# Optimization experiments

Hardware: AMD Instinct MI355X
Metric: run time of the kernel (lower is better)

## Reference

```python
import jax, jax.numpy as jnp
import numpy as np

B, N, D = 4, 2048, 512
H, DA, DL = 8, 64, 64  # heads, attention_dim, linear_dim
EPS = 1e-6


def _layer_norm(x, eps=EPS):
    # F.layer_norm with no affine params
    mu = jnp.mean(x, axis=-1, keepdims=True)
    var = jnp.var(x, axis=-1, keepdims=True)
    return (x - mu) * jax.lax.rsqrt(var + eps)


def setup_inputs() -> dict:
    key = jax.random.key(0)
    k1, k2, k3, k4 = jax.random.split(key, 4)
    x = jax.random.normal(k1, (B, N, D), dtype=jnp.float32)
    # causal (lower-triangular) valid-attention mask, float {0,1}, shape (B,1,N,N)
    attention_mask = jnp.broadcast_to(
        jnp.tril(jnp.ones((N, N), dtype=jnp.float32))[None, None], (B, 1, N, N)
    )
    # _uvqk: (D, 2*H*DL + 2*H*DA), init normal(0, 0.02)
    uvqk = 0.02 * jax.random.normal(k2, (D, 2 * H * DL + 2 * H * DA), dtype=jnp.float32)
    # _o: Linear(H*DL -> D), xavier uniform
    fan_in, fan_out = H * DL, D
    limit = float(np.sqrt(6.0 / (fan_in + fan_out)))
    o_weight = jax.random.uniform(k3, (fan_out, fan_in), dtype=jnp.float32, minval=-limit, maxval=limit)
    o_bias = jnp.zeros((D,), dtype=jnp.float32)
    return {"x": x, "attention_mask": attention_mask, "uvqk": uvqk,
            "o_weight": o_weight, "o_bias": o_bias}


def reference(x, attention_mask, uvqk, o_weight, o_bias):
    b, n, _ = x.shape
    normed_x = _layer_norm(x)
    mm = jax.nn.silu(normed_x @ uvqk)  # fused uvqk projection + silu
    u, v, q, k = jnp.split(mm, [H * DL, 2 * H * DL, 2 * H * DL + H * DA], axis=-1)
    qh = q.reshape(b, n, H, DA)
    kh = k.reshape(b, n, H, DA)
    vh = v.reshape(b, n, H, DL)
    # silu-activated (non-softmax) attention with mask
    qk = jnp.einsum('bnhd,bmhd->bhnm', qh, kh)
    qk = jax.nn.silu(qk) / n
    qk = qk * attention_mask  # (B,1,N,N) broadcast over heads
    attn = jnp.einsum('bhnm,bmhd->bnhd', qk, vh).reshape(b, n, H * DL)
    # gated norm + output proj + residual
    o_input = u * _layer_norm(attn)
    return o_input @ o_weight.T + o_bias + x
```

## Files before the change

### kernel.cpp

```cpp
#include <hip/hip_runtime.h>

typedef __bf16 bf16x8 __attribute__((ext_vector_type(8)));
typedef float f32x4 __attribute__((ext_vector_type(4)));
typedef float f32x16 __attribute__((ext_vector_type(16)));
typedef int i32x2 __attribute__((ext_vector_type(2)));

__device__ __forceinline__ unsigned short f2bf(float f) {
  return __builtin_bit_cast(unsigned short, (__bf16)f);
}
__device__ __forceinline__ float bfu2f(unsigned short b) {
  unsigned int u = ((unsigned int)b) << 16;
  return __builtin_bit_cast(float, u);
}
__device__ __forceinline__ float silu_f(float x) {
  return x * __builtin_amdgcn_rcpf(1.0f + __expf(-x));
}
__device__ __forceinline__ unsigned pk2(float a, float b) {
  return (unsigned)f2bf(a) | ((unsigned)f2bf(b) << 16);
}

template<int CPR, int NI, int SWZ>
__device__ __forceinline__ void stage16(const __bf16* __restrict__ g, int ld,
                                        __bf16* lds, int wave, int lane) {
#pragma unroll
  for (int t = 0; t < NI; ++t) {
    int cb = (wave * NI + t) * 64;
    int c = cb + lane;
    int row = c / CPR;
    int colb = (c % CPR) ^ (row & SWZ);
    __builtin_amdgcn_global_load_lds(
        (const __attribute__((address_space(1))) unsigned int*)(g + row * ld + colb * 8),
        (__attribute__((address_space(3))) unsigned int*)(lds + cb * 8),
        16, 0, 0);
  }
}

__global__ void k_prep(const float* __restrict__ x, __bf16* __restrict__ nx,
                       const float* __restrict__ ow, __bf16* __restrict__ owb,
                       const float* __restrict__ uvqk, __bf16* __restrict__ uvqkT) {
  int bid = blockIdx.x, tid = threadIdx.x;
  if (bid < 4096) {
    int t = tid & 127;
    int r = bid * 2 + (tid >> 7);
    int wave = tid >> 6;
    float4 v = ((const float4*)(x + (size_t)r * 512))[t];
    float s = v.x + v.y + v.z + v.w;
    float ss = v.x * v.x + v.y * v.y + v.z * v.z + v.w * v.w;
#pragma unroll
    for (int o = 32; o > 0; o >>= 1) { s += __shfl_down(s, o); ss += __shfl_down(ss, o); }
    __shared__ float red[4][2];
    if ((tid & 63) == 0) { red[wave][0] = s; red[wave][1] = ss; }
    __syncthreads();
    int rw = (wave >> 1) * 2;
    s = red[rw][0] + red[rw + 1][0];
    ss = red[rw][1] + red[rw + 1][1];
    float mu = s * (1.0f / 512.0f);
    float var = ss * (1.0f / 512.0f) - mu * mu;
    float rs = rsqrtf(var + 1e-6f);
    ushort4 o4;
    o4.x = f2bf((v.x - mu) * rs); o4.y = f2bf((v.y - mu) * rs);
    o4.z = f2bf((v.z - mu) * rs); o4.w = f2bf((v.w - mu) * rs);
    ((ushort4*)(nx + (size_t)r * 512))[t] = o4;
  } else if (bid < 4352) {
    int i = (bid - 4096) * 256 + tid;
    float4 v = ((const float4*)ow)[i];
    ushort4 o4;
    o4.x = f2bf(v.x); o4.y = f2bf(v.y); o4.z = f2bf(v.z); o4.w = f2bf(v.w);
    ((ushort4*)owb)[i] = o4;
  } else {
    __shared__ float tile[32][33];
    int bb = bid - 4352;
    int n0 = (bb & 63) * 32, k0 = (bb >> 6) * 32;
    int tx = tid & 31, ty = tid >> 5;
    for (int i = ty; i < 32; i += 8)
      tile[i][tx] = uvqk[(k0 + i) * 2048 + n0 + tx];
    __syncthreads();
    for (int i = ty; i < 32; i += 8)
      uvqkT[(n0 + i) * 512 + k0 + tx] = (__bf16)tile[tx][i];
  }
}

__global__ __launch_bounds__(256, 2) void k_proj(
    const __bf16* __restrict__ A, const __bf16* __restrict__ Bt,
    __bf16* __restrict__ u, __bf16* __restrict__ qn,
    __bf16* __restrict__ kn, __bf16* __restrict__ vt) {
  __shared__ __bf16 lds[32768];
  int tid = threadIdx.x, wave = tid >> 6, lane = tid & 63;
  int lr = lane & 15, lq = lane >> 4;
  int bn = blockIdx.x, bm = blockIdx.y;
  const __bf16* Ag = A + (size_t)bm * 128 * 512;
  const __bf16* Bg = Bt + (size_t)bn * 128 * 512;
  int wm = (wave >> 1) * 64, wn = (wave & 1) * 64;
  f32x4 acc[4][4] = {};
  stage16<8, 4, 7>(Ag, 512, lds, wave, lane);
  stage16<8, 4, 7>(Bg, 512, lds + 8192, wave, lane);
  asm volatile("s_waitcnt vmcnt(0)" ::: "memory");
  __builtin_amdgcn_sched_barrier(0);
  __builtin_amdgcn_s_barrier();
  __builtin_amdgcn_sched_barrier(0);
  int buf = 0;
  for (int t = 0; t < 8; ++t) {
    if (t + 1 < 8) {
      int nb = buf ^ 1;
      stage16<8, 4, 7>(Ag + (t + 1) * 64, 512, lds + nb * 16384, wave, lane);
      stage16<8, 4, 7>(Bg + (t + 1) * 64, 512, lds + nb * 16384 + 8192, wave, lane);
    }
    const __bf16* As = lds + buf * 16384;
    const __bf16* Bs = lds + buf * 16384 + 8192;
#pragma unroll
    for (int kk = 0; kk < 2; ++kk) {
      int b = kk * 4 + lq;
      bf16x8 a[4], bb[4];
#pragma unroll
      for (int i = 0; i < 4; ++i) {
        int row = wm + i * 16 + lr;
        a[i] = *(const bf16x8*)(As + row * 64 + ((b ^ (row & 7)) * 8));
      }
#pragma unroll
      for (int j = 0; j < 4; ++j) {
        int row = wn + j * 16 + lr;
        bb[j] = *(const bf16x8*)(Bs + row * 64 + ((b ^ (row & 7)) * 8));
      }
#pragma unroll
      for (int i = 0; i < 4; ++i)
#pragma unroll
        for (int j = 0; j < 4; ++j)
          acc[i][j] = __builtin_amdgcn_mfma_f32_16x16x32_bf16(a[i], bb[j], acc[i][j], 0, 0, 0);
    }
    asm volatile("s_waitcnt vmcnt(0)" ::: "memory");
    __builtin_amdgcn_sched_barrier(0);
    __builtin_amdgcn_s_barrier();
    __builtin_amdgcn_sched_barrier(0);
    buf ^= 1;
  }
  int seg = bn >> 2;
  int cb = (bn & 3) * 128 + wn;
  int rb0 = bm * 128 + wm + lq * 4;
  if (seg == 1) {
#pragma unroll
    for (int i = 0; i < 4; ++i) {
      int rb = rb0 + i * 16;
      int b = rb >> 11, n = rb & 2047;
#pragma unroll
      for (int j = 0; j < 4; ++j) {
        int c = cb + j * 16 + lr;
        ushort4 w;
        w.x = f2bf(silu_f(acc[i][j][0]) * (1.0f / 2048.0f));
        w.y = f2bf(silu_f(acc[i][j][1]) * (1.0f / 2048.0f));
        w.z = f2bf(silu_f(acc[i][j][2]) * (1.0f / 2048.0f));
        w.w = f2bf(silu_f(acc[i][j][3]) * (1.0f / 2048.0f));
        *(ushort4*)(vt + ((size_t)(b * 512 + c)) * 2048 + n) = w;
      }
    }
  } else {
    __bf16* dst = (seg == 0) ? u : ((seg == 2) ? qn : kn);
#pragma unroll
    for (int i = 0; i < 4; ++i) {
      int rb = rb0 + i * 16;
#pragma unroll
      for (int j = 0; j < 4; ++j) {
        int c = cb + j * 16 + lr;
#pragma unroll
        for (int rg = 0; rg < 4; ++rg)
          dst[(size_t)(rb + rg) * 512 + c] = (__bf16)silu_f(acc[i][j][rg]);
      }
    }
  }
}

template<bool DT>
__device__ __forceinline__ void attn_finish(
    const f32x16& s, int m0, int n0, int l31, int lh, int ms, bool natural,
    const __bf16* Vc, f32x16 po[2]) {
  unsigned pk[8];
#pragma unroll
  for (int q = 0; q < 8; ++q) {
    float p01[2];
#pragma unroll
    for (int h = 0; h < 2; ++h) {
      int r = 2 * q + h;
      float xx = s[r];
      float pv = xx * __builtin_amdgcn_rcpf(1.0f + __expf(-xx));
      if (DT) {
        int mrow = m0 + 4 * lh + (r & 3) + 8 * (r >> 2);
        if (mrow > n0 + l31) pv = 0.0f;
      }
      p01[h] = pv;
    }
    pk[q] = pk2(p01[0], p01[1]);
  }
  i32x2 r0 = __builtin_amdgcn_permlane32_swap((int)pk[0], (int)pk[2], false, false);
  i32x2 r1 = __builtin_amdgcn_permlane32_swap((int)pk[1], (int)pk[3], false, false);
  i32x2 r2 = __builtin_amdgcn_permlane32_swap((int)pk[4], (int)pk[6], false, false);
  i32x2 r3 = __builtin_amdgcn_permlane32_swap((int)pk[5], (int)pk[7], false, false);
  union { bf16x8 v; unsigned u[4]; } f0, f1;
  if (natural) {
    f0.u[0] = r0.x; f0.u[2] = r0.y; f0.u[1] = r1.x; f0.u[3] = r1.y;
    f1.u[0] = r2.x; f1.u[2] = r2.y; f1.u[1] = r3.x; f1.u[3] = r3.y;
  } else {
    f0.u[0] = r0.y; f0.u[2] = r0.x; f0.u[1] = r1.y; f0.u[3] = r1.x;
    f1.u[0] = r2.y; f1.u[2] = r2.x; f1.u[1] = r3.y; f1.u[3] = r3.x;
  }
  bf16x8 pf[2] = { f0.v, f1.v };
#pragma unroll
  for (int t2 = 0; t2 < 2; ++t2) {
#pragma unroll
    for (int idl = 0; idl < 2; ++idl) {
      int row = idl * 32 + l31;
      bf16x8 av = *(const bf16x8*)(Vc + row * 64 +
          (((ms * 4 + t2 * 2 + lh) ^ (row & 7)) * 8));
      po[idl] = __builtin_amdgcn_mfma_f32_32x32x16_bf16(av, pf[t2], po[idl], 0, 0, 0);
    }
  }
}

__global__ __launch_bounds__(256, 4) void k_attn(
    const __bf16* __restrict__ qn, const __bf16* __restrict__ kn,
    const __bf16* __restrict__ vt, __bf16* __restrict__ oa,
    __bf16* __restrict__ ob, __bf16* __restrict__ oc) {
  __shared__ __bf16 lds[16384];
  __bf16* Kb0 = lds;
  __bf16* Kb1 = lds + 4096;
  __bf16* Vb0 = lds + 8192;
  __bf16* Vb1 = lds + 12288;
  __bf16* bo = lds;

  int bh = blockIdx.x, p = blockIdx.y, z = blockIdx.z;
  int b = bh >> 3, hd = bh & 7;
  int tid = threadIdx.x, wave = tid >> 6, lane = tid & 63;
  int l31 = lane & 31, lh = lane >> 5;
  const __bf16* Kg = kn + (size_t)(b * 2048) * 512 + hd * 64;
  const __bf16* Vg = vt + (size_t)(b * 512 + hd * 64) * 2048;
  __bf16* Oz = (z == 0) ? oa : ((z == 1) ? ob : oc);

  i32x2 pr = __builtin_amdgcn_permlane32_swap(lh ? 10 : 11, lh ? 20 : 21, false, false);
  bool natural = (__builtin_amdgcn_readfirstlane(pr.x) == 11);

  for (int ph = 0; ph < 2; ++ph) {
    int t = ph ? (15 - p) : p;
    int T = 2 * t + 2;
    int mlo = z * T / 3;
    int cnt = (z + 1) * T / 3 - mlo;
    int n0 = t * 128 + wave * 32;
    if (ph) __syncthreads();
    const __bf16* Qg = qn + (size_t)(b * 2048 + n0 + l31) * 512 + hd * 64 + lh * 8;
    bf16x8 qf[4];
#pragma unroll
    for (int ks = 0; ks < 4; ++ks) qf[ks] = *(const bf16x8*)(Qg + ks * 16);
    if (cnt > 0) {
      stage16<8, 2, 7>(Kg + (size_t)mlo * 64 * 512, 512, Kb0, wave, lane);
      stage16<8, 2, 7>(Vg + mlo * 64, 2048, Vb0, wave, lane);
    }
    __syncthreads();

    f32x16 po[2] = {};

    for (int i = 0; i < cnt; ++i) {
      int mt = mlo + i;
      const __bf16* Kc = (i & 1) ? Kb1 : Kb0;
      const __bf16* Vc = (i & 1) ? Vb1 : Vb0;
      if (i + 1 < cnt) {
        __bf16* Kn_ = (i & 1) ? Kb0 : Kb1;
        __bf16* Vn_ = (i & 1) ? Vb0 : Vb1;
        stage16<8, 2, 7>(Kg + (size_t)(mt + 1) * 64 * 512, 512, Kn_, wave, lane);
        stage16<8, 2, 7>(Vg + (mt + 1) * 64, 2048, Vn_, wave, lane);
      }
#pragma unroll
      for (int ms = 0; ms < 2; ++ms) {
        int m0 = mt * 64 + ms * 32;
        if (m0 > n0) continue;
        f32x16 s = {};
#pragma unroll
        for (int ks = 0; ks < 4; ++ks) {
          int row = ms * 32 + l31;
          bf16x8 ak = *(const bf16x8*)(Kc + row * 64 + (((ks * 2 + lh) ^ (row & 7)) * 8));
          s = __builtin_amdgcn_mfma_f32_32x32x16_bf16(ak, qf[ks], s, 0, 0, 0);
        }
        if (m0 == n0) attn_finish<true>(s, m0, n0, l31, lh, ms, natural, Vc, po);
        else          attn_finish<false>(s, m0, n0, l31, lh, ms, natural, Vc, po);
      }
      __syncthreads();
    }

    {
      int nrow = wave * 32 + l31;
#pragma unroll
      for (int idl = 0; idl < 2; ++idl) {
#pragma unroll
        for (int g = 0; g < 4; ++g) {
          int dl0 = idl * 32 + g * 8 + lh * 4;
          int addr = nrow * 64 + ((((dl0 >> 3) ^ (nrow & 7)) << 3) | (dl0 & 7));
          ushort4 w;
          w.x = f2bf(po[idl][4 * g + 0]); w.y = f2bf(po[idl][4 * g + 1]);
          w.z = f2bf(po[idl][4 * g + 2]); w.w = f2bf(po[idl][4 * g + 3]);
          *(ushort4*)(bo + addr) = w;
        }
      }
    }
    __syncthreads();
    {
      int n = tid >> 1, cc = (tid & 1) * 32;
      __bf16* gdst = Oz + (size_t)(b * 2048 + t * 128 + n) * 512 + hd * 64 + cc;
#pragma unroll
      for (int kk2 = 0; kk2 < 4; ++kk2) {
        int dlb = cc + kk2 * 8;
        int a = n * 64 + (((dlb >> 3) ^ (n & 7)) << 3);
        *(uint4*)(gdst + kk2 * 8) = *(const uint4*)(bo + a);
      }
    }
  }
}

__global__ void k_oinput(const __bf16* __restrict__ oa, const __bf16* __restrict__ ob,
                         const __bf16* __restrict__ oc, const __bf16* __restrict__ u,
                         __bf16* __restrict__ oin) {
  int r = blockIdx.x, t = threadIdx.x;
  ushort4 a4 = ((const ushort4*)(oa + (size_t)r * 512))[t];
  ushort4 b4 = ((const ushort4*)(ob + (size_t)r * 512))[t];
  ushort4 c4 = ((const ushort4*)(oc + (size_t)r * 512))[t];
  float a0 = bfu2f(a4.x) + bfu2f(b4.x) + bfu2f(c4.x);
  float a1 = bfu2f(a4.y) + bfu2f(b4.y) + bfu2f(c4.y);
  float a2 = bfu2f(a4.z) + bfu2f(b4.z) + bfu2f(c4.z);
  float a3 = bfu2f(a4.w) + bfu2f(b4.w) + bfu2f(c4.w);
  float s = a0 + a1 + a2 + a3;
  float ss = a0 * a0 + a1 * a1 + a2 * a2 + a3 * a3;
#pragma unroll
  for (int o = 32; o > 0; o >>= 1) { s += __shfl_down(s, o); ss += __shfl_down(ss, o); }
  __shared__ float red[4];
  if ((t & 63) == 0) { red[(t >> 6) * 2] = s; red[(t >> 6) * 2 + 1] = ss; }
  __syncthreads();
  s = red[0] + red[2]; ss = red[1] + red[3];
  float mu = s * (1.0f / 512.0f);
  float var = ss * (1.0f / 512.0f) - mu * mu;
  float rs = rsqrtf(var + 1e-6f);
  ushort4 u4 = ((const ushort4*)(u + (size_t)r * 512))[t];
  ushort4 o4;
  o4.x = f2bf(bfu2f(u4.x) * (a0 - mu) * rs);
  o4.y = f2bf(bfu2f(u4.y) * (a1 - mu) * rs);
  o4.z = f2bf(bfu2f(u4.z) * (a2 - mu) * rs);
  o4.w = f2bf(bfu2f(u4.w) * (a3 - mu) * rs);
  ((ushort4*)(oin + (size_t)r * 512))[t] = o4;
}

__global__ __launch_bounds__(256, 3) void k_out(
    const __bf16* __restrict__ A, const __bf16* __restrict__ Bt,
    const float* __restrict__ bias, const float* __restrict__ x,
    float* __restrict__ out) {
  __shared__ __bf16 lds[24576];
  int tid = threadIdx.x, wave = tid >> 6, lane = tid & 63;
  int lr = lane & 15, lq = lane >> 4;
  int bn = blockIdx.x, bm = blockIdx.y;
  const __bf16* Ag = A + (size_t)bm * 64 * 512;
  const __bf16* Bg = Bt + (size_t)bn * 128 * 512;
  int wm = (wave >> 1) * 32, wn = (wave & 1) * 64;
  f32x4 acc[2][4] = {};
  stage16<8, 2, 7>(Ag, 512, lds, wave, lane);
  stage16<8, 4, 7>(Bg, 512, lds + 4096, wave, lane);
  asm volatile("s_waitcnt vmcnt(0)" ::: "memory");
  __builtin_amdgcn_sched_barrier(0);
  __builtin_amdgcn_s_barrier();
  __builtin_amdgcn_sched_barrier(0);
  int buf = 0;
  for (int t = 0; t < 8; ++t) {
    if (t + 1 < 8) {
      int nb = buf ^ 1;
      stage16<8, 2, 7>(Ag + (t + 1) * 64, 512, lds + nb * 12288, wave, lane);
      stage16<8, 4, 7>(Bg + (t + 1) * 64, 512, lds + nb * 12288 + 4096, wave, lane);
    }
    const __bf16* As = lds + buf * 12288;
    const __bf16* Bs = lds + buf * 12288 + 4096;
#pragma unroll
    for (int kk = 0; kk < 2; ++kk) {
      int b = kk * 4 + lq;
      bf16x8 a[2], bb[4];
#pragma unroll
      for (int i = 0; i < 2; ++i) {
        int row = wm + i * 16 + lr;
        a[i] = *(const bf16x8*)(As + row * 64 + ((b ^ (row & 7)) * 8));
      }
#pragma unroll
      for (int j = 0; j < 4; ++j) {
        int row = wn + j * 16 + lr;
        bb[j] = *(const bf16x8*)(Bs + row * 64 + ((b ^ (row & 7)) * 8));
      }
#pragma unroll
      for (int i = 0; i < 2; ++i)
#pragma unroll
        for (int j = 0; j < 4; ++j)
          acc[i][j] = __builtin_amdgcn_mfma_f32_16x16x32_bf16(a[i], bb[j], acc[i][j], 0, 0, 0);
    }
    asm volatile("s_waitcnt vmcnt(0)" ::: "memory");
    __builtin_amdgcn_sched_barrier(0);
    __builtin_amdgcn_s_barrier();
    __builtin_amdgcn_sched_barrier(0);
    buf ^= 1;
  }
  int cb = bn * 128 + wn;
  int rb0 = bm * 64 + wm + lq * 4;
#pragma unroll
  for (int j = 0; j < 4; ++j) {
    int c = cb + j * 16 + lr;
    float bv = bias[c];
#pragma unroll
    for (int i = 0; i < 2; ++i) {
      int rb = rb0 + i * 16;
#pragma unroll
      for (int rg = 0; rg < 4; ++rg) {
        size_t idx = (size_t)(rb + rg) * 512 + c;
        out[idx] = acc[i][j][rg] + bv + x[idx];
      }
    }
  }
}

extern "C" void kernel_launch(void* const* d_in, const int* in_sizes, int n_in,
                              void* d_out, int out_size, void* d_ws, size_t ws_size,
                              hipStream_t stream) {
  const float* x = (const float*)d_in[0];
  const float* uvqk = (const float*)d_in[2];
  const float* ow = (const float*)d_in[3];
  const float* obias = (const float*)d_in[4];
  float* out = (float*)d_out;

  char* w = (char*)d_ws;
  const size_t MB8 = 8u * 1024 * 1024;
  __bf16* nx    = (__bf16*)(w);
  __bf16* u     = (__bf16*)(w + MB8);
  __bf16* qn    = (__bf16*)(w + 2 * MB8);
  __bf16* kn    = (__bf16*)(w + 3 * MB8);
  __bf16* vt    = (__bf16*)(w + 4 * MB8);
  __bf16* uvqkT = (__bf16*)(w + 5 * MB8);
  __bf16* owb   = (__bf16*)(w + 5 * MB8 + 2097152);
  __bf16* Oa    = nx;
  __bf16* Ob    = (__bf16*)d_out;
  __bf16* Oc    = (__bf16*)d_out + (size_t)8192 * 512;
  __bf16* o_in  = qn;

  k_prep<<<5376, 256, 0, stream>>>(x, nx, ow, owb, uvqk, uvqkT);
  k_proj<<<dim3(16, 64), 256, 0, stream>>>(nx, uvqkT, u, qn, kn, vt);
  k_attn<<<dim3(32, 8, 3), 256, 0, stream>>>(qn, kn, vt, Oa, Ob, Oc);
  k_oinput<<<8192, 128, 0, stream>>>(Oa, Ob, Oc, u, o_in);
  k_out<<<dim3(4, 128), 256, 0, stream>>>(o_in, owb, obias, x, out);
}
```

Measured before the change: 196.9 us.

## Fuse gated layer-norm o-input computation into output projection GEMM

Adds a fused kernel that sums the three attention partial outputs, applies the row layer norm and u-gating, and writes the bf16 A tile straight into LDS before running the output-projection GEMM with residual. This drops the separate k_oinput launch and the write and re-read of o_in through global memory. The partial buffers move from d_out into extra workspace when it is large enough, with the old path kept as a fallback. In exchange the row tile shrinks to 32, so each block reads the partials twice and the gating work is repeated across the 4 column blocks.

```diff
diff --git a/kernel.cpp b/kernel.cpp
--- a/kernel.cpp
+++ b/kernel.cpp
@@ -413,6 +413,120 @@
   }
 }
 
+__global__ __launch_bounds__(256, 2) void k_out_fused(
+    const __bf16* __restrict__ oa, const __bf16* __restrict__ ob,
+    const __bf16* __restrict__ oc, const __bf16* __restrict__ u,
+    const __bf16* __restrict__ Bt, const float* __restrict__ bias,
+    const float* __restrict__ x, float* __restrict__ out) {
+  __shared__ __bf16 lds[32768];
+  int tid = threadIdx.x, wave = tid >> 6, lane = tid & 63;
+  int lr = lane & 15, lq = lane >> 4;
+  int bn = blockIdx.x, bm = blockIdx.y;
+  const __bf16* Bg = Bt + (size_t)bn * 128 * 512;
+  int wn = wave * 32;
+
+  {
+    int r = tid >> 3, q = tid & 7;
+    size_t R = (size_t)(bm * 32 + r) * 512;
+    float s = 0.f, ss = 0.f;
+#pragma unroll
+    for (int j = 0; j < 8; ++j) {
+      int c = q * 8 + j * 64;
+      uint4 a4 = *(const uint4*)(oa + R + c);
+      uint4 b4 = *(const uint4*)(ob + R + c);
+      uint4 c4 = *(const uint4*)(oc + R + c);
+#pragma unroll
+      for (int e = 0; e < 4; ++e) {
+        unsigned aw = ((const unsigned*)&a4)[e], bw = ((const unsigned*)&b4)[e],
+                 cw = ((const unsigned*)&c4)[e];
+        float v0 = bfu2f((unsigned short)aw) + bfu2f((unsigned short)bw) + bfu2f((unsigned short)cw);
+        float v1 = bfu2f((unsigned short)(aw >> 16)) + bfu2f((unsigned short)(bw >> 16)) + bfu2f((unsigned short)(cw >> 16));
+        s += v0 + v1; ss += v0 * v0 + v1 * v1;
+      }
+    }
+    s += __shfl_xor(s, 1); ss += __shfl_xor(ss, 1);
+    s += __shfl_xor(s, 2); ss += __shfl_xor(ss, 2);
+    s += __shfl_xor(s, 4); ss += __shfl_xor(ss, 4);
+    float mu = s * (1.0f / 512.0f);
+    float var = ss * (1.0f / 512.0f) - mu * mu;
+    float rs = rsqrtf(var + 1e-6f);
+#pragma unroll
+    for (int j = 0; j < 8; ++j) {
+      int c = q * 8 + j * 64;
+      uint4 a4 = *(const uint4*)(oa + R + c);
+      uint4 b4 = *(const uint4*)(ob + R + c);
+      uint4 c4 = *(const uint4*)(oc + R + c);
+      uint4 u4 = *(const uint4*)(u + R + c);
+      uint4 w;
+#pragma unroll
+      for (int e = 0; e < 4; ++e) {
+        unsigned aw = ((const unsigned*)&a4)[e], bw = ((const unsigned*)&b4)[e],
+                 cw = ((const unsigned*)&c4)[e], uw = ((const unsigned*)&u4)[e];
+        float v0 = bfu2f((unsigned short)aw) + bfu2f((unsigned short)bw) + bfu2f((unsigned short)cw);
+        float v1 = bfu2f((unsigned short)(aw >> 16)) + bfu2f((unsigned short)(bw >> 16)) + bfu2f((unsigned short)(cw >> 16));
+        float g0 = bfu2f((unsigned short)uw) * (v0 - mu) * rs;
+        float g1 = bfu2f((unsigned short)(uw >> 16)) * (v1 - mu) * rs;
+        ((unsigned*)&w)[e] = pk2(g0, g1);
+      }
+      *(uint4*)(lds + j * 2048 + r * 64 + ((q ^ (r & 7)) * 8)) = w;
+    }
+  }
+  stage16<8, 4, 7>(Bg, 512, lds + 16384, wave, lane);
+  __syncthreads();
+
+  f32x4 acc[2][2] = {};
+  int buf = 0;
+  for (int t = 0; t < 8; ++t) {
+    if (t + 1 < 8) {
+      int nb = buf ^ 1;
+      stage16<8, 4, 7>(Bg + (t + 1) * 64, 512, lds + 16384 + nb * 8192, wave, lane);
+    }
+    const __bf16* As = lds + t * 2048;
+    const __bf16* Bs = lds + 16384 + buf * 8192;
+#pragma unroll
+    for (int kk = 0; kk < 2; ++kk) {
+      int b = kk * 4 + lq;
+      bf16x8 a[2], bb[2];
+#pragma unroll
+      for (int i = 0; i < 2; ++i) {
+        int row = i * 16 + lr;
+        a[i] = *(const bf16x8*)(As + row * 64 + ((b ^ (row & 7)) * 8));
+      }
+#pragma unroll
+      for (int j = 0; j < 2; ++j) {
+        int row = wn + j * 16 + lr;
+        bb[j] = *(const bf16x8*)(Bs + row * 64 + ((b ^ (row & 7)) * 8));
+      }
+#pragma unroll
+      for (int i = 0; i < 2; ++i)
+#pragma unroll
+        for (int j = 0; j < 2; ++j)
+          acc[i][j] = __builtin_amdgcn_mfma_f32_16x16x32_bf16(a[i], bb[j], acc[i][j], 0, 0, 0);
+    }
+    asm volatile("s_waitcnt vmcnt(0)" ::: "memory");
+    __builtin_amdgcn_sched_barrier(0);
+    __builtin_amdgcn_s_barrier();
+    __builtin_amdgcn_sched_barrier(0);
+    buf ^= 1;
+  }
+  int cb = bn * 128 + wn;
+  int rb0 = bm * 32 + lq * 4;
+#pragma unroll
+  for (int j = 0; j < 2; ++j) {
+    int c = cb + j * 16 + lr;
+    float bv = bias[c];
+#pragma unroll
+    for (int i = 0; i < 2; ++i) {
+      int rb = rb0 + i * 16;
+#pragma unroll
+      for (int rg = 0; rg < 4; ++rg) {
+        size_t idx = (size_t)(rb + rg) * 512 + c;
+        out[idx] = acc[i][j][rg] + bv + x[idx];
+      }
+    }
+  }
+}
+
 extern "C" void kernel_launch(void* const* d_in, const int* in_sizes, int n_in,
                               void* d_out, int out_size, void* d_ws, size_t ws_size,
                               hipStream_t stream) {
@@ -431,14 +545,23 @@
   __bf16* vt    = (__bf16*)(w + 4 * MB8);
   __bf16* uvqkT = (__bf16*)(w + 5 * MB8);
   __bf16* owb   = (__bf16*)(w + 5 * MB8 + 2097152);
+  size_t tail = 5 * MB8 + 2097152 + 524288;
   __bf16* Oa    = nx;
-  __bf16* Ob    = (__bf16*)d_out;
-  __bf16* Oc    = (__bf16*)d_out + (size_t)8192 * 512;
-  __bf16* o_in  = qn;
 
   k_prep<<<5376, 256, 0, stream>>>(x, nx, ow, owb, uvqk, uvqkT);
   k_proj<<<dim3(16, 64), 256, 0, stream>>>(nx, uvqkT, u, qn, kn, vt);
-  k_attn<<<dim3(32, 8, 3), 256, 0, stream>>>(qn, kn, vt, Oa, Ob, Oc);
-  k_oinput<<<8192, 128, 0, stream>>>(Oa, Ob, Oc, u, o_in);
-  k_out<<<dim3(4, 128), 256, 0, stream>>>(o_in, owb, obias, x, out);
-}
+
+  if (ws_size >= tail + 2 * MB8) {
+    __bf16* Ob = (__bf16*)(w + tail);
+    __bf16* Oc = (__bf16*)(w + tail + MB8);
+    k_attn<<<dim3(32, 8, 3), 256, 0, stream>>>(qn, kn, vt, Oa, Ob, Oc);
+    k_out_fused<<<dim3(4, 256), 256, 0, stream>>>(Oa, Ob, Oc, u, owb, obias, x, out);
+  } else {
+    __bf16* Ob = (__bf16*)d_out;
+    __bf16* Oc = (__bf16*)d_out + (size_t)8192 * 512;
+    __bf16* o_in = qn;
+    k_attn<<<dim3(32, 8, 3), 256, 0, stream>>>(qn, kn, vt, Oa, Ob, Oc);
+    k_oinput<<<8192, 128, 0, stream>>>(Oa, Ob, Oc, u, o_in);
+    k_out<<<dim3(4, 128), 256, 0, stream>>>(o_in, owb, obias, x, out);
+  }
+}
```

Result: slower. 210.3 us (+6.8%).

## Use 128-wide KV tiles and a 2-way key split in attention

Applied to the files above, without the earlier changes.

The attention kernel now stages 128-row K and V tiles per iteration instead of 64, and splits the key range two ways instead of three. LDS use doubles to 64KB and launch bounds drop to 2 blocks per CU. The aim is fewer barriers and staging rounds per tile and less partial-output traffic, since k_oinput now sums two partial buffers instead of three. The cost is lower occupancy, fewer blocks to balance the triangular workload, and a longer serial loop per block.

```diff
diff --git a/kernel.cpp b/kernel.cpp
--- a/kernel.cpp
+++ b/kernel.cpp
@@ -207,22 +207,18 @@
 #pragma unroll
     for (int idl = 0; idl < 2; ++idl) {
       int row = idl * 32 + l31;
-      bf16x8 av = *(const bf16x8*)(Vc + row * 64 +
+      bf16x8 av = *(const bf16x8*)(Vc + row * 128 +
           (((ms * 4 + t2 * 2 + lh) ^ (row & 7)) * 8));
       po[idl] = __builtin_amdgcn_mfma_f32_32x32x16_bf16(av, pf[t2], po[idl], 0, 0, 0);
     }
   }
 }
 
-__global__ __launch_bounds__(256, 4) void k_attn(
+__global__ __launch_bounds__(256, 2) void k_attn(
     const __bf16* __restrict__ qn, const __bf16* __restrict__ kn,
     const __bf16* __restrict__ vt, __bf16* __restrict__ oa,
-    __bf16* __restrict__ ob, __bf16* __restrict__ oc) {
-  __shared__ __bf16 lds[16384];
-  __bf16* Kb0 = lds;
-  __bf16* Kb1 = lds + 4096;
-  __bf16* Vb0 = lds + 8192;
-  __bf16* Vb1 = lds + 12288;
+    __bf16* __restrict__ ob) {
+  __shared__ __bf16 lds[32768];
   __bf16* bo = lds;
 
   int bh = blockIdx.x, p = blockIdx.y, z = blockIdx.z;
@@ -231,16 +227,16 @@
   int l31 = lane & 31, lh = lane >> 5;
   const __bf16* Kg = kn + (size_t)(b * 2048) * 512 + hd * 64;
   const __bf16* Vg = vt + (size_t)(b * 512 + hd * 64) * 2048;
-  __bf16* Oz = (z == 0) ? oa : ((z == 1) ? ob : oc);
+  __bf16* Oz = z ? ob : oa;
 
   i32x2 pr = __builtin_amdgcn_permlane32_swap(lh ? 10 : 11, lh ? 20 : 21, false, false);
   bool natural = (__builtin_amdgcn_readfirstlane(pr.x) == 11);
 
   for (int ph = 0; ph < 2; ++ph) {
     int t = ph ? (15 - p) : p;
-    int T = 2 * t + 2;
-    int mlo = z * T / 3;
-    int cnt = (z + 1) * T / 3 - mlo;
+    int T = t + 1;
+    int mlo = z * T / 2;
+    int cnt = (z + 1) * T / 2 - mlo;
     int n0 = t * 128 + wave * 32;
     if (ph) __syncthreads();
     const __bf16* Qg = qn + (size_t)(b * 2048 + n0 + l31) * 512 + hd * 64 + lh * 8;
@@ -248,8 +244,8 @@
 #pragma unroll
     for (int ks = 0; ks < 4; ++ks) qf[ks] = *(const bf16x8*)(Qg + ks * 16);
     if (cnt > 0) {
-      stage16<8, 2, 7>(Kg + (size_t)mlo * 64 * 512, 512, Kb0, wave, lane);
-      stage16<8, 2, 7>(Vg + mlo * 64, 2048, Vb0, wave, lane);
+      stage16<8, 4, 7>(Kg + (size_t)mlo * 128 * 512, 512, lds, wave, lane);
+      stage16<16, 4, 7>(Vg + mlo * 128, 2048, lds + 16384, wave, lane);
     }
     __syncthreads();
 
@@ -257,17 +253,17 @@
 
     for (int i = 0; i < cnt; ++i) {
       int mt = mlo + i;
-      const __bf16* Kc = (i & 1) ? Kb1 : Kb0;
-      const __bf16* Vc = (i & 1) ? Vb1 : Vb0;
+      const __bf16* Kc = lds + (i & 1) * 8192;
+      const __bf16* Vc = lds + 16384 + (i & 1) * 8192;
       if (i + 1 < cnt) {
-        __bf16* Kn_ = (i & 1) ? Kb0 : Kb1;
-        __bf16* Vn_ = (i & 1) ? Vb0 : Vb1;
-        stage16<8, 2, 7>(Kg + (size_t)(mt + 1) * 64 * 512, 512, Kn_, wave, lane);
-        stage16<8, 2, 7>(Vg + (mt + 1) * 64, 2048, Vn_, wave, lane);
-      }
-#pragma unroll
-      for (int ms = 0; ms < 2; ++ms) {
-        int m0 = mt * 64 + ms * 32;
+        __bf16* Kn_ = lds + ((i & 1) ^ 1) * 8192;
+        __bf16* Vn_ = lds + 16384 + ((i & 1) ^ 1) * 8192;
+        stage16<8, 4, 7>(Kg + (size_t)(mt + 1) * 128 * 512, 512, Kn_, wave, lane);
+        stage16<16, 4, 7>(Vg + (mt + 1) * 128, 2048, Vn_, wave, lane);
+      }
+#pragma unroll
+      for (int ms = 0; ms < 4; ++ms) {
+        int m0 = mt * 128 + ms * 32;
         if (m0 > n0) continue;
         f32x16 s = {};
 #pragma unroll
@@ -312,16 +308,14 @@
 }
 
 __global__ void k_oinput(const __bf16* __restrict__ oa, const __bf16* __restrict__ ob,
-                         const __bf16* __restrict__ oc, const __bf16* __restrict__ u,
-                         __bf16* __restrict__ oin) {
+                         const __bf16* __restrict__ u, __bf16* __restrict__ oin) {
   int r = blockIdx.x, t = threadIdx.x;
   ushort4 a4 = ((const ushort4*)(oa + (size_t)r * 512))[t];
   ushort4 b4 = ((const ushort4*)(ob + (size_t)r * 512))[t];
-  ushort4 c4 = ((const ushort4*)(oc + (size_t)r * 512))[t];
-  float a0 = bfu2f(a4.x) + bfu2f(b4.x) + bfu2f(c4.x);
-  float a1 = bfu2f(a4.y) + bfu2f(b4.y) + bfu2f(c4.y);
-  float a2 = bfu2f(a4.z) + bfu2f(b4.z) + bfu2f(c4.z);
-  float a3 = bfu2f(a4.w) + bfu2f(b4.w) + bfu2f(c4.w);
+  float a0 = bfu2f(a4.x) + bfu2f(b4.x);
+  float a1 = bfu2f(a4.y) + bfu2f(b4.y);
+  float a2 = bfu2f(a4.z) + bfu2f(b4.z);
+  float a3 = bfu2f(a4.w) + bfu2f(b4.w);
   float s = a0 + a1 + a2 + a3;
   float ss = a0 * a0 + a1 * a1 + a2 * a2 + a3 * a3;
 #pragma unroll
@@ -433,12 +427,11 @@
   __bf16* owb   = (__bf16*)(w + 5 * MB8 + 2097152);
   __bf16* Oa    = nx;
   __bf16* Ob    = (__bf16*)d_out;
-  __bf16* Oc    = (__bf16*)d_out + (size_t)8192 * 512;
   __bf16* o_in  = qn;
 
   k_prep<<<5376, 256, 0, stream>>>(x, nx, ow, owb, uvqk, uvqkT);
   k_proj<<<dim3(16, 64), 256, 0, stream>>>(nx, uvqkT, u, qn, kn, vt);
-  k_attn<<<dim3(32, 8, 3), 256, 0, stream>>>(qn, kn, vt, Oa, Ob, Oc);
-  k_oinput<<<8192, 128, 0, stream>>>(Oa, Ob, Oc, u, o_in);
+  k_attn<<<dim3(32, 8, 2), 256, 0, stream>>>(qn, kn, vt, Oa, Ob);
+  k_oinput<<<8192, 128, 0, stream>>>(Oa, Ob, u, o_in);
   k_out<<<dim3(4, 128), 256, 0, stream>>>(o_in, owb, obias, x, out);
 }
```

After: 193.5 us (median of 2 runs). About the same (-1.7%).
